# Kernel optimization log

Hardware: AMD Instinct MI355X
Metric: run time of the kernel (lower is better)

The kernel has to match this reference:

```python
import jax, jax.numpy as jnp
import numpy as np
import math

B, T, O, C, H, L, V, S = 4, 1024, 128, 1024, 16, 4, 32000, 4096
D = C // H
PAD = 0


def setup_inputs() -> dict:
    key = jax.random.key(0)
    ks = jax.random.split(key, 16)
    r = lambda i, shape, s=0.02: jax.random.normal(ks[i], shape, jnp.float32) * s
    return {
        "tokens_w": jax.random.randint(ks[0], (B, T), 0, V).astype(jnp.int32),
        "pos_offset": 0,
        "mem": jax.random.normal(ks[1], (B, O, C), jnp.float32),
        "ssum": jax.random.normal(ks[2], (B, C), jnp.float32),
        "tok_emb_w": r(3, (V, C)),
        "pos_emb_w": r(4, (S, C)),
        "mem_w": r(5, (C, C)), "mem_b": jnp.zeros((C,), jnp.float32),
        "memln_s": jnp.ones((C,), jnp.float32), "memln_b": jnp.zeros((C,), jnp.float32),
        "alpha_p": jnp.zeros((C,), jnp.float32),
        "sum_w": r(6, (C, C)),
        "ln1_s": jnp.ones((L, C), jnp.float32), "ln1_b": jnp.zeros((L, C), jnp.float32),
        "Wq": r(7, (L, C, C)), "bq": jnp.zeros((L, C), jnp.float32),
        "Wk": r(8, (L, C, C)), "bk": jnp.zeros((L, C), jnp.float32),
        "Wv": r(9, (L, C, C)), "bv": jnp.zeros((L, C), jnp.float32),
        "Wo": r(10, (L, C, C)), "bo": jnp.zeros((L, C), jnp.float32),
        "ln2_s": jnp.ones((L, C), jnp.float32), "ln2_b": jnp.zeros((L, C), jnp.float32),
        "W1": r(11, (L, C, 4 * C)), "b1": jnp.zeros((L, 4 * C), jnp.float32),
        "W2": r(12, (L, 4 * C, C)), "b2": jnp.zeros((L, C), jnp.float32),
        "fln_s": jnp.ones((C,), jnp.float32), "fln_b": jnp.zeros((C,), jnp.float32),
        "head_w": r(13, (C, V)), "head_b": jnp.zeros((V,), jnp.float32),
        "lam_p": jnp.zeros((C,), jnp.float32),
    }


def _ln(x, s, b, eps=1e-6):
    mu = jnp.mean(x, -1, keepdims=True)
    var = jnp.mean((x - mu) ** 2, -1, keepdims=True)
    return (x - mu) * jax.lax.rsqrt(var + eps) * s + b


def reference(tokens_w, pos_offset, mem, ssum, tok_emb_w, pos_emb_w, mem_w, mem_b,
              memln_s, memln_b, alpha_p, sum_w, ln1_s, ln1_b, Wq, bq, Wk, bk, Wv, bv,
              Wo, bo, ln2_s, ln2_b, W1, b1, W2, b2, fln_s, fln_b, head_w, head_b, lam_p):
    Bx, Tx = tokens_w.shape
    tok = tok_emb_w[tokens_w]                                   # [B,T,C]
    pos_ids = jnp.clip(jnp.arange(Tx, dtype=jnp.int32) + pos_offset, 0, S - 1)
    x = tok + pos_emb_w[pos_ids][None, :, :]
    # memory adapter + norm (saved-before-masking memory state)
    m2 = _ln(mem @ mem_w + mem_b, memln_s, memln_b)             # [B,O,C]
    alpha = jax.nn.sigmoid(alpha_p)
    x = x + ((ssum @ sum_w) * alpha[None, :])[:, None, :]
    # boolean mask: memory tokens always visible + causal window + key padding
    causal = jnp.concatenate([jnp.ones((Tx, O), bool),
                              jnp.tril(jnp.ones((Tx, Tx), bool))], axis=1)[None, None]
    key_ok = jnp.concatenate([jnp.ones((Bx, O), bool), tokens_w != PAD], axis=1)
    mask = causal & key_ok[:, None, None, :]                    # [B,1,T,O+T]
    scale = 1.0 / math.sqrt(D)
    for i in range(L):
        kv = jnp.concatenate([m2, x], axis=1)                   # [B,O+T,C]
        h = _ln(x, ln1_s[i], ln1_b[i])
        q = (h @ Wq[i] + bq[i]).reshape(Bx, Tx, H, D)
        k = (kv @ Wk[i] + bk[i]).reshape(Bx, O + Tx, H, D)
        v = (kv @ Wv[i] + bv[i]).reshape(Bx, O + Tx, H, D)
        att = jnp.einsum('bqhd,bkhd->bhqk', q, k) * scale
        att = jnp.where(mask, att, -1e9)
        p = jax.nn.softmax(att, axis=-1)
        o = jnp.einsum('bhqk,bkhd->bqhd', p, v).reshape(Bx, Tx, C)
        x = x + (o @ Wo[i] + bo[i])
        h = _ln(x, ln2_s[i], ln2_b[i])
        x = x + (jax.nn.gelu(h @ W1[i] + b1[i]) @ W2[i] + b2[i])
    x = _ln(x, fln_s, fln_b)
    new_mem = x[:, -O:, :]
    m = (tokens_w != PAD).astype(x.dtype)
    x = x * m[:, :, None]
    logits = x @ head_w + head_b                                # [B,T,V]
    summary = jnp.sum(x * m[:, :, None], axis=1) / (jnp.sum(m, axis=1, keepdims=True) + 1e-6)
    lam = jax.nn.sigmoid(lam_p)
    new_ssum = ssum * lam[None, :] + summary * (1.0 - lam[None, :])
    return (new_mem, new_ssum, logits)
```

## Files before the change

kernel.cpp:

```cpp
#include <hip/hip_runtime.h>
#include <hip/hip_bf16.h>

typedef __bf16 bf16_t;
typedef __bf16 bf16x8 __attribute__((ext_vector_type(8)));
typedef __bf16 bf16x4 __attribute__((ext_vector_type(4)));
typedef float f32x4 __attribute__((ext_vector_type(4)));

#define NB 4
#define NT 1024
#define NO 128
#define NC 1024
#define NH 16
#define NL 4
#define NV 32000
#define NS 4096
#define ND 64
#define NTK (NO + NT)

#define GLOAD_LDS16(g, l) __builtin_amdgcn_global_load_lds( \
    (__attribute__((address_space(1))) void*)(g), \
    (__attribute__((address_space(3))) void*)(l), 16, 0, 0)

#define EXP2F(x) __builtin_amdgcn_exp2f(x)

__device__ __forceinline__ float sigmoidf_(float x) { return 1.0f / (1.0f + __expf(-x)); }

#define EPI_F32  0
#define EPI_ADD  1
#define EPI_GELU 2
#define EPI_QKV  3
#define EPI_KV   4

template<int EPI>
__global__ __launch_bounds__(512) void gemm8p(
    const bf16_t* __restrict__ A, const bf16_t* __restrict__ Bt,
    const float* __restrict__ bias, float* __restrict__ outF,
    bf16_t* __restrict__ outB, int M, int N, int K, int ldo, int gm)
{
    __shared__ bf16_t sm[65536];
    const int tid = threadIdx.x;
    const int w = tid >> 6, lane = tid & 63;
    const int wr = w >> 2, wc = w & 3;
    const int lr = lane & 15, lk = lane >> 4;
    const int nwg = gridDim.x;
    const int bid = blockIdx.x;
    const int xcd = bid & 7, base = bid >> 3;
    const int qq = nwg >> 3, rr = nwg & 7;
    int wg = (xcd < rr ? xcd * (qq + 1) : rr * (qq + 1) + (xcd - rr) * qq) + base;
    const int nnt = N >> 8;
    const int gsz = gm * nnt;
    const int g = wg / gsz, r2 = wg - g * gsz;
    const int ntl = r2 / gm, mt = g * gm + (r2 - ntl * gm);
    const int bm = mt << 8, bn = ntl << 8;
    const bf16_t* Ab = A + (size_t)bm * K;
    const bf16_t* Bb = Bt + (size_t)bn * K;
    const int srow = tid >> 3;
    const int scol = ((tid & 7) ^ (srow & 7)) << 3;
    const int nk = K >> 6;
    f32x4 acc[8][4] = {};

    auto STAGE = [&](int b, int kt, int h) {
        const bf16_t* gsrc = (h < 2) ? Ab : Bb;
        const int half = h & 1;
        char* lbase = (char*)(sm + ((h < 2) ? 0 : 32768) + b * 16384 + half * 8192);
        #pragma unroll
        for (int i = 0; i < 2; ++i) {
            GLOAD_LDS16(gsrc + (size_t)(half * 128 + i * 64 + srow) * K + kt * 64 + scol,
                        lbase + (i * 512 + tid) * 16);
        }
    };

    #pragma unroll
    for (int h = 0; h < 4; ++h) STAGE(0, 0, h);
    asm volatile("s_waitcnt vmcnt(0)" ::: "memory");
    __builtin_amdgcn_s_barrier();

    for (int kt = 0; kt < nk; ++kt) {
        const int curb = kt & 1;
        const bool dostage = (kt + 1) < nk;
        const char* Abase = (const char*)(sm + curb * 16384);
        const char* Bbase = (const char*)(sm + 32768 + curb * 16384);

        if (dostage) {
            STAGE(curb ^ 1, kt + 1, 0);
            STAGE(curb ^ 1, kt + 1, 1);
            asm volatile("s_waitcnt vmcnt(4)" ::: "memory");
        } else {
            asm volatile("s_waitcnt vmcnt(0)" ::: "memory");
        }
        __builtin_amdgcn_s_barrier();

        bf16x8 bfr[4][2];
        #pragma unroll
        for (int n = 0; n < 4; ++n)
            #pragma unroll
            for (int ks = 0; ks < 2; ++ks) {
                const int row = wc * 64 + n * 16 + lr;
                bfr[n][ks] = *(const bf16x8*)(Bbase + row * 128 + ((((ks << 2) + lk) ^ (row & 7)) << 4));
            }
        bf16x8 af[4][2];
        #pragma unroll
        for (int m = 0; m < 4; ++m)
            #pragma unroll
            for (int ks = 0; ks < 2; ++ks) {
                const int row = wr * 128 + m * 16 + lr;
                af[m][ks] = *(const bf16x8*)(Abase + row * 128 + ((((ks << 2) + lk) ^ (row & 7)) << 4));
            }
        asm volatile("s_waitcnt lgkmcnt(0)" ::: "memory");
        __builtin_amdgcn_sched_barrier(0);
        __builtin_amdgcn_s_setprio(1);
        #pragma unroll
        for (int m = 0; m < 4; ++m)
            #pragma unroll
            for (int n = 0; n < 4; ++n)
                #pragma unroll
                for (int ks = 0; ks < 2; ++ks)
                    acc[m][n] = __builtin_amdgcn_mfma_f32_16x16x32_bf16(
                        af[m][ks], bfr[n][ks], acc[m][n], 0, 0, 0);
        __builtin_amdgcn_s_setprio(0);

        if (dostage) {
            STAGE(curb ^ 1, kt + 1, 2);
            STAGE(curb ^ 1, kt + 1, 3);
        }
        bf16x8 ag[4][2];
        #pragma unroll
        for (int m = 0; m < 4; ++m)
            #pragma unroll
            for (int ks = 0; ks < 2; ++ks) {
                const int row = wr * 128 + 64 + m * 16 + lr;
                ag[m][ks] = *(const bf16x8*)(Abase + row * 128 + ((((ks << 2) + lk) ^ (row & 7)) << 4));
            }
        asm volatile("s_waitcnt lgkmcnt(0)" ::: "memory");
        __builtin_amdgcn_sched_barrier(0);
        __builtin_amdgcn_s_setprio(1);
        #pragma unroll
        for (int m = 0; m < 4; ++m)
            #pragma unroll
            for (int n = 0; n < 4; ++n)
                #pragma unroll
                for (int ks = 0; ks < 2; ++ks)
                    acc[4 + m][n] = __builtin_amdgcn_mfma_f32_16x16x32_bf16(
                        ag[m][ks], bfr[n][ks], acc[4 + m][n], 0, 0, 0);
        __builtin_amdgcn_s_setprio(0);
        __builtin_amdgcn_s_barrier();
    }

    float bv4[4];
    #pragma unroll
    for (int n = 0; n < 4; ++n) bv4[n] = bias[bn + wc * 64 + n * 16 + lr];
    #pragma unroll
    for (int m = 0; m < 8; ++m) {
        #pragma unroll
        for (int j = 0; j < 4; ++j) {
            const int row = bm + wr * 128 + m * 16 + lk * 4 + j;
            #pragma unroll
            for (int n = 0; n < 4; ++n) {
                const int col = bn + wc * 64 + n * 16 + lr;
                float v = acc[m][n][j] + bv4[n];
                if constexpr (EPI == 0) {
                    __builtin_nontemporal_store(v, &outF[(size_t)row * ldo + col]);
                } else {
                    float u = 1.5957691216057308f * (v + 0.044715f * v * v * v);
                    float g_ = v / (1.0f + __expf(-u));
                    outB[(size_t)row * ldo + col] = (bf16_t)g_;
                }
            }
        }
    }
}

template<int EPI>
__device__ __forceinline__ void gemm128_body(
    bf16_t* sm, int bid, int nwg,
    const bf16_t* __restrict__ A, const bf16_t* __restrict__ Bt,
    const float* __restrict__ bias, const float* __restrict__ bias2,
    float* __restrict__ outF, bf16_t* __restrict__ outB, bf16_t* __restrict__ outB2,
    int M, int N, int K, int p0, int ldo, int gm)
{
    char* smb = (char*)sm;
    const int tid = threadIdx.x;
    const int w = tid >> 6, lane = tid & 63;
    const int wr = w >> 1, wc = w & 1;
    const int lr = lane & 15, lk = lane >> 4;
    const int xcd = bid & 7, base = bid >> 3;
    const int qq = nwg >> 3, rr = nwg & 7;
    int wg = (xcd < rr ? xcd * (qq + 1) : rr * (qq + 1) + (xcd - rr) * qq) + base;
    const int nnt = N >> 7;
    const int gsz = gm * nnt;
    const int g = wg / gsz, r2 = wg - g * gsz;
    const int ntl = r2 / gm, mt = g * gm + (r2 - ntl * gm);
    const int bm = mt << 7, bn = ntl << 7;
    const bf16_t* Ab = A + (size_t)bm * K;
    const bf16_t* Bb = Bt + (size_t)bn * K;
    const int srow = tid >> 3;
    const int scol = ((tid & 7) ^ (srow & 7)) << 3;
    const int nk = K >> 6;
    f32x4 acc[4][4] = {};

    auto STAGE = [&](int b, int kt, int h) {
        const bf16_t* gsrc = h ? Bb : Ab;
        char* lbase = smb + h * 32768 + b * 16384;
        #pragma unroll
        for (int i = 0; i < 4; ++i) {
            GLOAD_LDS16(gsrc + (size_t)(i * 32 + srow) * K + kt * 64 + scol,
                        lbase + (i * 256 + tid) * 16);
        }
    };

    STAGE(0, 0, 0); STAGE(0, 0, 1);
    asm volatile("s_waitcnt vmcnt(0)" ::: "memory");
    __builtin_amdgcn_s_barrier();

    for (int kt = 0; kt < nk; ++kt) {
        const int curb = kt & 1;
        const bool dostage = (kt + 1) < nk;
        const char* Abase = smb + curb * 16384;
        const char* Bbase = smb + 32768 + curb * 16384;

        if (dostage) {
            STAGE(curb ^ 1, kt + 1, 0);
            asm volatile("s_waitcnt vmcnt(4)" ::: "memory");
        } else {
            asm volatile("s_waitcnt vmcnt(0)" ::: "memory");
        }
        __builtin_amdgcn_s_barrier();

        bf16x8 bfr[4][2];
        #pragma unroll
        for (int n = 0; n < 4; ++n)
            #pragma unroll
            for (int ks_ = 0; ks_ < 2; ++ks_) {
                const int row = wc * 64 + n * 16 + lr;
                bfr[n][ks_] = *(const bf16x8*)(Bbase + row * 128 + ((((ks_ << 2) + lk) ^ (row & 7)) << 4));
            }
        bf16x8 af[4];
        #pragma unroll
        for (int m = 0; m < 4; ++m) {
            const int row = wr * 64 + m * 16 + lr;
            af[m] = *(const bf16x8*)(Abase + row * 128 + (((lk) ^ (row & 7)) << 4));
        }
        asm volatile("s_waitcnt lgkmcnt(0)" ::: "memory");
        __builtin_amdgcn_sched_barrier(0);
        __builtin_amdgcn_s_setprio(1);
        #pragma unroll
        for (int m = 0; m < 4; ++m)
            #pragma unroll
            for (int n = 0; n < 4; ++n)
                acc[m][n] = __builtin_amdgcn_mfma_f32_16x16x32_bf16(
                    af[m], bfr[n][0], acc[m][n], 0, 0, 0);
        __builtin_amdgcn_s_setprio(0);

        if (dostage) STAGE(curb ^ 1, kt + 1, 1);
        bf16x8 ag[4];
        #pragma unroll
        for (int m = 0; m < 4; ++m) {
            const int row = wr * 64 + m * 16 + lr;
            ag[m] = *(const bf16x8*)(Abase + row * 128 + (((4 + lk) ^ (row & 7)) << 4));
        }
        asm volatile("s_waitcnt lgkmcnt(0)" ::: "memory");
        __builtin_amdgcn_sched_barrier(0);
        __builtin_amdgcn_s_setprio(1);
        #pragma unroll
        for (int m = 0; m < 4; ++m)
            #pragma unroll
            for (int n = 0; n < 4; ++n)
                acc[m][n] = __builtin_amdgcn_mfma_f32_16x16x32_bf16(
                    ag[m], bfr[n][1], acc[m][n], 0, 0, 0);
        __builtin_amdgcn_s_setprio(0);
        __builtin_amdgcn_s_barrier();
    }

    #pragma unroll
    for (int m = 0; m < 4; ++m) {
        #pragma unroll
        for (int j = 0; j < 4; ++j) {
            const int row = bm + wr * 64 + m * 16 + lk * 4 + j;
            int b_ = 0, t_ = 0;
            if constexpr (EPI == EPI_QKV || EPI == EPI_KV) { b_ = row / p0; t_ = row % p0; }
            #pragma unroll
            for (int n = 0; n < 4; ++n) {
                const int col = bn + wc * 64 + n * 16 + lr;
                if constexpr (EPI == EPI_F32) {
                    float v = acc[m][n][j] + bias[col];
                    __builtin_nontemporal_store(v, &outF[(size_t)row * ldo + col]);
                } else if constexpr (EPI == EPI_ADD) {
                    float v = acc[m][n][j] + bias[col];
                    outF[(size_t)row * ldo + col] += v;
                } else if constexpr (EPI == EPI_GELU) {
                    float v = acc[m][n][j] + bias[col];
                    float u = 1.5957691216057308f * (v + 0.044715f * v * v * v);
                    float g_ = v / (1.0f + __expf(-u));
                    outB[(size_t)row * ldo + col] = (bf16_t)g_;
                } else if constexpr (EPI == EPI_QKV) {
                    float v = acc[m][n][j] + bias[col];
                    int h = col >> 6, d = col & 63;
                    outB[(((size_t)b_ * NH + h) * p0 + t_) * ND + d] = (bf16_t)v;
                } else if constexpr (EPI == EPI_KV) {
                    if (col < NC) {
                        float v = acc[m][n][j] + bias[col];
                        int h = col >> 6, d = col & 63;
                        outB[(((size_t)b_ * NH + h) * NTK + t_) * ND + d] = (bf16_t)v;
                    } else {
                        int c2_ = col - NC;
                        float v = acc[m][n][j] + bias2[c2_];
                        int h = c2_ >> 6, d = c2_ & 63;
                        outB2[(((size_t)b_ * NH + h) * ND + d) * NTK + t_] = (bf16_t)v;
                    }
                }
            }
        }
    }
}

template<int EPI>
__global__ __launch_bounds__(256) void gemm128(
    const bf16_t* __restrict__ A, const bf16_t* __restrict__ Bt,
    const float* __restrict__ bias, const float* __restrict__ bias2,
    float* __restrict__ outF, bf16_t* __restrict__ outB, bf16_t* __restrict__ outB2,
    int M, int N, int K, int p0, int ldo, int gm)
{
    __shared__ bf16_t sm[32768];
    gemm128_body<EPI>(sm, blockIdx.x, gridDim.x, A, Bt, bias, bias2,
                      outF, outB, outB2, M, N, K, p0, ldo, gm);
}

__global__ __launch_bounds__(256) void qkv_fused(
    const bf16_t* __restrict__ hbuf, const bf16_t* __restrict__ kvbuf,
    const bf16_t* __restrict__ wtq, const bf16_t* __restrict__ wtkv,
    const float* __restrict__ bq, const float* __restrict__ bk,
    const float* __restrict__ bv,
    bf16_t* __restrict__ qbuf, bf16_t* __restrict__ kbuf, bf16_t* __restrict__ vtbuf)
{
    __shared__ bf16_t sm[32768];
    if (blockIdx.x < 256) {
        gemm128_body<EPI_QKV>(sm, blockIdx.x, 256, hbuf, wtq, bq, nullptr,
                              nullptr, qbuf, nullptr, NB * NT, NC, NC, NT, 0, 8);
    } else {
        gemm128_body<EPI_KV>(sm, blockIdx.x - 256, 576, kvbuf, wtkv, bk, bv,
                             nullptr, kbuf, vtbuf, NB * NTK, 2 * NC, NC, NTK, 0, 6);
    }
}

template<int EPI>
__global__ __launch_bounds__(256) void gemm_bt(
    const bf16_t* __restrict__ A, const bf16_t* __restrict__ Bt,
    const float* __restrict__ bias, const float* __restrict__ bias2,
    float* __restrict__ outF, bf16_t* __restrict__ outB, bf16_t* __restrict__ outB2,
    int M, int N, int K, int p0, int ldo, int gm)
{
    __shared__ bf16_t lA[128 * 32];
    __shared__ bf16_t lB[128 * 32];
    const int tid = threadIdx.x;
    const int nwg = gridDim.x;
    const int bid = blockIdx.x;
    const int xcd = bid & 7, base = bid >> 3;
    const int qq = nwg >> 3, rr = nwg & 7;
    int wg = (xcd < rr ? xcd * (qq + 1) : rr * (qq + 1) + (xcd - rr) * qq) + base;
    const int nnt = N >> 7;
    const int gsz = gm * nnt;
    const int g = wg / gsz, r2 = wg - g * gsz;
    const int ntl = r2 / gm, mt = g * gm + (r2 - ntl * gm);
    const int bm = mt * 128, bn = ntl * 128;
    const bf16_t* Ab = A + (size_t)bm * K;
    const bf16_t* Bb = Bt + (size_t)bn * K;
    const int wave = tid >> 6, lane = tid & 63;
    const int wr = wave >> 1, wc = wave & 1;
    const int lr = lane & 15, lk = lane >> 4;
    f32x4 acc[4][4] = {};
    const int nk = K >> 5;
    const int c1 = tid, c2 = tid + 256;
    for (int kt = 0; kt < nk; ++kt) {
        __syncthreads();
        const bf16_t* Abk = Ab + kt * 32;
        const bf16_t* Bbk = Bb + kt * 32;
        GLOAD_LDS16(Abk + (size_t)(c1 >> 2) * K + (c1 & 3) * 8, (char*)lA + c1 * 16);
        GLOAD_LDS16(Abk + (size_t)(c2 >> 2) * K + (c2 & 3) * 8, (char*)lA + c2 * 16);
        GLOAD_LDS16(Bbk + (size_t)(c1 >> 2) * K + (c1 & 3) * 8, (char*)lB + c1 * 16);
        GLOAD_LDS16(Bbk + (size_t)(c2 >> 2) * K + (c2 & 3) * 8, (char*)lB + c2 * 16);
        __syncthreads();
        bf16x8 af[4], bfr[4];
        #pragma unroll
        for (int m = 0; m < 4; ++m)
            af[m] = *(const bf16x8*)&lA[(wr * 64 + m * 16 + lr) * 32 + lk * 8];
        #pragma unroll
        for (int n = 0; n < 4; ++n)
            bfr[n] = *(const bf16x8*)&lB[(wc * 64 + n * 16 + lr) * 32 + lk * 8];
        #pragma unroll
        for (int m = 0; m < 4; ++m)
            #pragma unroll
            for (int n = 0; n < 4; ++n)
                acc[m][n] = __builtin_amdgcn_mfma_f32_16x16x32_bf16(af[m], bfr[n], acc[m][n], 0, 0, 0);
    }
    #pragma unroll
    for (int m = 0; m < 4; ++m) {
        #pragma unroll
        for (int j = 0; j < 4; ++j) {
            const int row = bm + wr * 64 + m * 16 + lk * 4 + j;
            #pragma unroll
            for (int n = 0; n < 4; ++n) {
                const int col = bn + wc * 64 + n * 16 + lr;
                if constexpr (EPI == EPI_F32) {
                    float v = acc[m][n][j] + bias[col];
                    __builtin_nontemporal_store(v, &outF[(size_t)row * ldo + col]);
                }
            }
        }
    }
}

__device__ __forceinline__ void tc_body(
    const float* __restrict__ W, bf16_t* __restrict__ Wt,
    int K, int N, int k0, int n0, int t)
{
    __shared__ float tile[64][65];
    #pragma unroll
    for (int i = 0; i < 4; ++i) {
        const int idx = t + i * 256;
        const int r = idx >> 4, c4 = (idx & 15) << 2;
        const float4 v = *(const float4*)(W + (size_t)(k0 + r) * N + n0 + c4);
        tile[r][c4 + 0] = v.x; tile[r][c4 + 1] = v.y;
        tile[r][c4 + 2] = v.z; tile[r][c4 + 3] = v.w;
    }
    __syncthreads();
    #pragma unroll
    for (int i = 0; i < 4; ++i) {
        const int idx = t + i * 256;
        const int r = idx >> 4, c4 = (idx & 15) << 2;
        bf16x4 o = {(bf16_t)tile[c4 + 0][r], (bf16_t)tile[c4 + 1][r],
                    (bf16_t)tile[c4 + 2][r], (bf16_t)tile[c4 + 3][r]};
        *(bf16x4*)(Wt + (size_t)(n0 + r) * K + k0 + c4) = o;
    }
}

__global__ __launch_bounds__(256) void transpose_cast(
    const float* __restrict__ W, bf16_t* __restrict__ Wt, int K, int N)
{
    tc_body(W, Wt, K, N, blockIdx.x << 6, blockIdx.y << 6, threadIdx.x);
}

__device__ __forceinline__ void ln3_body(
    int row, const float* __restrict__ X, const float* __restrict__ sw,
    const float* __restrict__ bw, bf16_t* __restrict__ outB,
    bf16_t* __restrict__ outB2)
{
    const int t = threadIdx.x;
    const float4 v = ((const float4*)(X + (size_t)row * NC))[t];
    float s1 = v.x + v.y + v.z + v.w;
    float s2 = v.x * v.x + v.y * v.y + v.z * v.z + v.w * v.w;
    #pragma unroll
    for (int off = 32; off > 0; off >>= 1) { s1 += __shfl_xor(s1, off); s2 += __shfl_xor(s2, off); }
    __shared__ float rs1[4], rs2[4];
    if ((t & 63) == 0) { rs1[t >> 6] = s1; rs2[t >> 6] = s2; }
    __syncthreads();
    s1 = rs1[0] + rs1[1] + rs1[2] + rs1[3];
    s2 = rs2[0] + rs2[1] + rs2[2] + rs2[3];
    const float mu = s1 * (1.0f / NC);
    const float var = s2 * (1.0f / NC) - mu * mu;
    const float rstd = rsqrtf(var + 1e-6f);
    const int c = t * 4;
    const float4 sv = ((const float4*)sw)[t];
    const float4 bv = ((const float4*)bw)[t];
    float y0 = (v.x - mu) * rstd * sv.x + bv.x;
    float y1 = (v.y - mu) * rstd * sv.y + bv.y;
    float y2 = (v.z - mu) * rstd * sv.z + bv.z;
    float y3 = (v.w - mu) * rstd * sv.w + bv.w;
    bf16x4 o = {(bf16_t)y0, (bf16_t)y1, (bf16_t)y2, (bf16_t)y3};
    *(bf16x4*)(outB + (size_t)row * NC + c) = o;
    const int b_ = row >> 10, t_ = row & 1023;
    bf16x4 o2 = {(bf16_t)v.x, (bf16_t)v.y, (bf16_t)v.z, (bf16_t)v.w};
    *(bf16x4*)(outB2 + ((size_t)b_ * NTK + NO + t_) * NC + c) = o2;
}

__global__ __launch_bounds__(256) void prep_layer(
    const float* __restrict__ Wq, const float* __restrict__ Wk,
    const float* __restrict__ Wv, const float* __restrict__ Wo,
    const float* __restrict__ W1, const float* __restrict__ W2,
    bf16_t* __restrict__ wtq, bf16_t* __restrict__ wtkv,
    bf16_t* __restrict__ wto, bf16_t* __restrict__ wt1, bf16_t* __restrict__ wt2,
    const float* __restrict__ X, const float* __restrict__ ln1s,
    const float* __restrict__ ln1b, bf16_t* __restrict__ hbuf,
    bf16_t* __restrict__ kvbuf)
{
    const int bid = blockIdx.x;
    if (bid >= 3072) {
        ln3_body(bid - 3072, X, ln1s, ln1b, hbuf, kvbuf);
        return;
    }
    const float* W; bf16_t* Wt; int K, N, k0, n0;
    if (bid < 1024) {
        const int which = bid >> 8, r = bid & 255;
        K = NC; N = NC;
        k0 = (r & 15) << 6; n0 = (r >> 4) << 6;
        W  = (which == 0) ? Wq : (which == 1) ? Wk : (which == 2) ? Wv : Wo;
        Wt = (which == 0) ? wtq : (which == 1) ? wtkv
           : (which == 2) ? (wtkv + (size_t)NC * NC) : wto;
    } else if (bid < 2048) {
        const int r = bid - 1024;
        K = NC; N = 4 * NC;
        k0 = (r & 15) << 6; n0 = (r >> 4) << 6;
        W = W1; Wt = wt1;
    } else {
        const int r = bid - 2048;
        K = 4 * NC; N = NC;
        k0 = (r & 63) << 6; n0 = (r >> 6) << 6;
        W = W2; Wt = wt2;
    }
    tc_body(W, Wt, K, N, k0, n0, threadIdx.x);
}

template<int MODE>
__global__ __launch_bounds__(256) void ln_row(
    const float* __restrict__ X, const float* __restrict__ sw,
    const float* __restrict__ bw, float* __restrict__ outF,
    bf16_t* __restrict__ outB, bf16_t* __restrict__ outB2)
{
    const int row = blockIdx.x;
    const int t = threadIdx.x;
    const float4 v = ((const float4*)(X + (size_t)row * NC))[t];
    float s1 = v.x + v.y + v.z + v.w;
    float s2 = v.x * v.x + v.y * v.y + v.z * v.z + v.w * v.w;
    #pragma unroll
    for (int off = 32; off > 0; off >>= 1) { s1 += __shfl_xor(s1, off); s2 += __shfl_xor(s2, off); }
    __shared__ float rs1[4], rs2[4];
    if ((t & 63) == 0) { rs1[t >> 6] = s1; rs2[t >> 6] = s2; }
    __syncthreads();
    s1 = rs1[0] + rs1[1] + rs1[2] + rs1[3];
    s2 = rs2[0] + rs2[1] + rs2[2] + rs2[3];
    const float mu = s1 * (1.0f / NC);
    const float var = s2 * (1.0f / NC) - mu * mu;
    const float rstd = rsqrtf(var + 1e-6f);
    const int c = t * 4;
    const float4 sv = ((const float4*)sw)[t];
    const float4 bv = ((const float4*)bw)[t];
    float y0 = (v.x - mu) * rstd * sv.x + bv.x;
    float y1 = (v.y - mu) * rstd * sv.y + bv.y;
    float y2 = (v.z - mu) * rstd * sv.z + bv.z;
    float y3 = (v.w - mu) * rstd * sv.w + bv.w;
    size_t dst;
    if constexpr (MODE == 1) dst = ((size_t)(row / NO) * NTK + (row % NO)) * NC + c;
    else dst = (size_t)row * NC + c;
    bf16x4 o = {(bf16_t)y0, (bf16_t)y1, (bf16_t)y2, (bf16_t)y3};
    *(bf16x4*)(outB + dst) = o;
}

__global__ __launch_bounds__(256) void ln_final(
    const float* __restrict__ X, const float* __restrict__ sw,
    const float* __restrict__ bw, const int* __restrict__ tokens,
    bf16_t* __restrict__ xm, float* __restrict__ outMem)
{
    const int row = blockIdx.x;
    const int t = threadIdx.x;
    const float4 v = ((const float4*)(X + (size_t)row * NC))[t];
    float s1 = v.x + v.y + v.z + v.w;
    float s2 = v.x * v.x + v.y * v.y + v.z * v.z + v.w * v.w;
    #pragma unroll
    for (int off = 32; off > 0; off >>= 1) { s1 += __shfl_xor(s1, off); s2 += __shfl_xor(s2, off); }
    __shared__ float rs1[4], rs2[4];
    if ((t & 63) == 0) { rs1[t >> 6] = s1; rs2[t >> 6] = s2; }
    __syncthreads();
    s1 = rs1[0] + rs1[1] + rs1[2] + rs1[3];
    s2 = rs2[0] + rs2[1] + rs2[2] + rs2[3];
    const float mu = s1 * (1.0f / NC);
    const float var = s2 * (1.0f / NC) - mu * mu;
    const float rstd = rsqrtf(var + 1e-6f);
    const int c = t * 4;
    const float4 sv = ((const float4*)sw)[t];
    const float4 bv = ((const float4*)bw)[t];
    float y0 = (v.x - mu) * rstd * sv.x + bv.x;
    float y1 = (v.y - mu) * rstd * sv.y + bv.y;
    float y2 = (v.z - mu) * rstd * sv.z + bv.z;
    float y3 = (v.w - mu) * rstd * sv.w + bv.w;
    const bool ok = tokens[row] != 0;
    bf16x4 o;
    if (ok) { o = (bf16x4){(bf16_t)y0, (bf16_t)y1, (bf16_t)y2, (bf16_t)y3}; }
    else    { o = (bf16x4){(bf16_t)0.f, (bf16_t)0.f, (bf16_t)0.f, (bf16_t)0.f}; }
    *(bf16x4*)(xm + (size_t)row * NC + c) = o;
    const int b_ = row >> 10, t_ = row & 1023;
    if (t_ >= NT - NO) {
        float4 f; f.x = y0; f.y = y1; f.z = y2; f.w = y3;
        *(float4*)(outMem + ((size_t)b_ * NO + (t_ - (NT - NO))) * NC + c) = f;
    }
}

#define QKSCALE 0.1803368801111204f

__global__ __launch_bounds__(256) void attn_kernel(
    const bf16_t* __restrict__ Q, const bf16_t* __restrict__ Kb,
    const bf16_t* __restrict__ Vt, const int* __restrict__ tokens,
    bf16_t* __restrict__ Ob)
{
    const int bh = blockIdx.x;
    const int b = bh >> 4, h = bh & 15;
    const int w = threadIdx.x >> 6;
    const int lane = threadIdx.x & 63;
    const int yt = gridDim.y - 1 - blockIdx.y;
    const int q0 = (yt << 7) + (w << 5);
    const int lr = lane & 15, lk = lane >> 4;
    const bf16_t* Qp = Q + ((size_t)bh * NT + q0) * ND;
    bf16x8 qf[2][2];
    #pragma unroll
    for (int qs = 0; qs < 2; ++qs) {
        qf[qs][0] = *(const bf16x8*)(Qp + (qs * 16 + lr) * ND + lk * 8);
        qf[qs][1] = *(const bf16x8*)(Qp + (qs * 16 + lr) * ND + 32 + lk * 8);
    }
    const bf16_t* Kbase = Kb + (size_t)bh * NTK * ND;
    const bf16_t* Vbase = Vt + (size_t)bh * ND * NTK;
    const int* tokb = tokens + b * NT;
    float mrow[2][4] = {{-1e30f, -1e30f, -1e30f, -1e30f}, {-1e30f, -1e30f, -1e30f, -1e30f}};
    float lsum[2][4] = {};
    f32x4 acc[2][4] = {};
    __shared__ bf16_t pb[4][2][16 * 64];
    const int kmax = NO + q0 + 32;
    for (int k0 = 0; k0 < kmax; k0 += 64) {
        f32x4 st[2][4] = {};
        __builtin_amdgcn_s_setprio(1);
        #pragma unroll
        for (int nt = 0; nt < 4; ++nt) {
            const bf16_t* Kp = Kbase + (size_t)(k0 + nt * 16 + lr) * ND + lk * 8;
            bf16x8 kf0 = *(const bf16x8*)(Kp);
            bf16x8 kf1 = *(const bf16x8*)(Kp + 32);
            #pragma unroll
            for (int qs = 0; qs < 2; ++qs) {
                st[qs][nt] = __builtin_amdgcn_mfma_f32_16x16x32_bf16(qf[qs][0], kf0, st[qs][nt], 0, 0, 0);
                st[qs][nt] = __builtin_amdgcn_mfma_f32_16x16x32_bf16(qf[qs][1], kf1, st[qs][nt], 0, 0, 0);
            }
        }
        __builtin_amdgcn_s_setprio(0);
        #pragma unroll
        for (int qs = 0; qs < 2; ++qs) {
            char* pbq = (char*)pb[w][qs];
            float sc[4][4];
            float tmax[4] = {-1e30f, -1e30f, -1e30f, -1e30f};
            #pragma unroll
            for (int nt = 0; nt < 4; ++nt) {
                const int key = k0 + nt * 16 + lr;
                const int kt = key - NO;
                const int kts = kt < 0 ? 0 : kt;
                const bool keyok = (kt < 0) | (tokb[kts] != 0);
                #pragma unroll
                for (int j = 0; j < 4; ++j) {
                    const int qrow = q0 + qs * 16 + lk * 4 + j;
                    const bool ok = keyok && (kt <= qrow);
                    const float s = ok ? st[qs][nt][j] * QKSCALE : -1e9f;
                    sc[nt][j] = s;
                    tmax[j] = fmaxf(tmax[j], s);
                }
            }
            #pragma unroll
            for (int off = 1; off < 16; off <<= 1)
                #pragma unroll
                for (int j = 0; j < 4; ++j) tmax[j] = fmaxf(tmax[j], __shfl_xor(tmax[j], off));
            float resc[4], p[4][4], psum[4] = {0.f, 0.f, 0.f, 0.f};
            #pragma unroll
            for (int j = 0; j < 4; ++j) {
                const float mnew = fmaxf(mrow[qs][j], tmax[j]);
                resc[j] = EXP2F(mrow[qs][j] - mnew);
                mrow[qs][j] = mnew;
            }
            #pragma unroll
            for (int nt = 0; nt < 4; ++nt)
                #pragma unroll
                for (int j = 0; j < 4; ++j) { p[nt][j] = EXP2F(sc[nt][j] - mrow[qs][j]); psum[j] += p[nt][j]; }
            #pragma unroll
            for (int off = 1; off < 16; off <<= 1)
                #pragma unroll
                for (int j = 0; j < 4; ++j) psum[j] += __shfl_xor(psum[j], off);
            #pragma unroll
            for (int j = 0; j < 4; ++j) lsum[qs][j] = lsum[qs][j] * resc[j] + psum[j];
            #pragma unroll
            for (int dt = 0; dt < 4; ++dt)
                #pragma unroll
                for (int j = 0; j < 4; ++j) acc[qs][dt][j] *= resc[j];
            #pragma unroll
            for (int nt = 0; nt < 4; ++nt)
                #pragma unroll
                for (int j = 0; j < 4; ++j) {
                    const int row = lk * 4 + j;
                    const int byt = (row << 7) + ((((nt << 4) + lr) << 1) ^ ((row & 7) << 4));
                    *(bf16_t*)(pbq + byt) = (bf16_t)p[nt][j];
                }
        }
        const int swz = (lr & 7) << 4;
        bf16x8 pa[2][2];
        #pragma unroll
        for (int qs = 0; qs < 2; ++qs) {
            const char* pbq = (const char*)pb[w][qs];
            pa[qs][0] = *(const bf16x8*)(pbq + ((lr << 7) + (((lk << 4)) ^ swz)));
            pa[qs][1] = *(const bf16x8*)(pbq + ((lr << 7) + ((64 + (lk << 4)) ^ swz)));
        }
        __builtin_amdgcn_s_setprio(1);
        #pragma unroll
        for (int dt = 0; dt < 4; ++dt) {
            const bf16_t* Vp = Vbase + (size_t)(dt * 16 + lr) * NTK + k0 + lk * 8;
            bf16x8 vf0 = *(const bf16x8*)(Vp);
            bf16x8 vf1 = *(const bf16x8*)(Vp + 32);
            #pragma unroll
            for (int qs = 0; qs < 2; ++qs) {
                acc[qs][dt] = __builtin_amdgcn_mfma_f32_16x16x32_bf16(pa[qs][0], vf0, acc[qs][dt], 0, 0, 0);
                acc[qs][dt] = __builtin_amdgcn_mfma_f32_16x16x32_bf16(pa[qs][1], vf1, acc[qs][dt], 0, 0, 0);
            }
        }
        __builtin_amdgcn_s_setprio(0);
    }
    #pragma unroll
    for (int qs = 0; qs < 2; ++qs)
        #pragma unroll
        for (int dt = 0; dt < 4; ++dt)
            #pragma unroll
            for (int j = 0; j < 4; ++j)
                Ob[((size_t)b * NT + q0 + qs * 16 + lk * 4 + j) * NC + h * ND + dt * 16 + lr] =
                    (bf16_t)(acc[qs][dt][j] / lsum[qs][j]);
}

__global__ __launch_bounds__(256) void sum_proj_kernel(
    const float* __restrict__ ssum, const float* __restrict__ sumw,
    const float* __restrict__ alpha, float* __restrict__ add)
{
    const int b = blockIdx.y;
    const int c = blockIdx.x * 256 + threadIdx.x;
    float a = 0.f;
    for (int k = 0; k < NC; ++k) a += ssum[b * NC + k] * sumw[(size_t)k * NC + c];
    add[b * NC + c] = a * sigmoidf_(alpha[c]);
}

__global__ __launch_bounds__(256) void embed_kernel(
    const int* __restrict__ tokens, const int* __restrict__ posoff,
    const float* __restrict__ tokw, const float* __restrict__ posw,
    const float* __restrict__ add, float* __restrict__ X)
{
    const int bt = blockIdx.x;
    const int b = bt >> 10, t = bt & 1023;
    const int c = threadIdx.x * 4;
    const int tok = tokens[bt];
    int p = t + posoff[0];
    p = p < 0 ? 0 : (p > NS - 1 ? NS - 1 : p);
    const float4 tv = *(const float4*)(tokw + (size_t)tok * NC + c);
    const float4 pv = *(const float4*)(posw + (size_t)p * NC + c);
    const float4 av = *(const float4*)(add + b * NC + c);
    float4 o;
    o.x = tv.x + pv.x + av.x; o.y = tv.y + pv.y + av.y;
    o.z = tv.z + pv.z + av.z; o.w = tv.w + pv.w + av.w;
    *(float4*)(X + (size_t)bt * NC + c) = o;
}

__global__ __launch_bounds__(256) void cast_f32_bf16_kernel(
    const float* __restrict__ in, bf16_t* __restrict__ out)
{
    const size_t i = ((size_t)blockIdx.x * 256 + threadIdx.x) * 4;
    const float4 v = *(const float4*)(in + i);
    bf16x4 o = {(bf16_t)v.x, (bf16_t)v.y, (bf16_t)v.z, (bf16_t)v.w};
    *(bf16x4*)(out + i) = o;
}

__global__ __launch_bounds__(256) void sumpart_kernel(
    const bf16_t* __restrict__ XM, float* __restrict__ sbuf)
{
    const int b = blockIdx.z;
    const int c = blockIdx.x * 256 + threadIdx.x;
    const int t0 = blockIdx.y * 64;
    float a = 0.f;
    for (int t = t0; t < t0 + 64; ++t)
        a += (float)XM[((size_t)b * NT + t) * NC + c];
    atomicAdd(&sbuf[b * NC + c], a);
}

__global__ __launch_bounds__(256) void ssum_out_kernel(
    const float* __restrict__ sbuf, const int* __restrict__ tokens,
    const float* __restrict__ ssum, const float* __restrict__ lamp, float* __restrict__ out)
{
    const int b = blockIdx.y;
    const int c = blockIdx.x * 256 + threadIdx.x;
    int cnt = 0;
    for (int t = 0; t < NT; ++t) cnt += (tokens[b * NT + t] != 0);
    const float summary = sbuf[b * NC + c] / ((float)cnt + 1e-6f);
    const float lam = sigmoidf_(lamp[c]);
    out[b * NC + c] = ssum[b * NC + c] * lam + summary * (1.0f - lam);
}

extern "C" void kernel_launch(void* const* d_in, const int* in_sizes, int n_in,
                              void* d_out, int out_size, void* d_ws, size_t ws_size,
                              hipStream_t stream)
{
    (void)in_sizes; (void)n_in; (void)out_size; (void)ws_size;
    const int*   tokens   = (const int*)d_in[0];
    const int*   posoff   = (const int*)d_in[1];
    const float* mem      = (const float*)d_in[2];
    const float* ssum     = (const float*)d_in[3];
    const float* tok_emb  = (const float*)d_in[4];
    const float* pos_emb  = (const float*)d_in[5];
    const float* mem_w    = (const float*)d_in[6];
    const float* mem_b    = (const float*)d_in[7];
    const float* memln_s  = (const float*)d_in[8];
    const float* memln_b  = (const float*)d_in[9];
    const float* alpha_p  = (const float*)d_in[10];
    const float* sum_w    = (const float*)d_in[11];
    const float* ln1_s    = (const float*)d_in[12];
    const float* ln1_b    = (const float*)d_in[13];
    const float* Wq       = (const float*)d_in[14];
    const float* bq       = (const float*)d_in[15];
    const float* Wk       = (const float*)d_in[16];
    const float* bk       = (const float*)d_in[17];
    const float* Wv       = (const float*)d_in[18];
    const float* bv       = (const float*)d_in[19];
    const float* Wo       = (const float*)d_in[20];
    const float* bo       = (const float*)d_in[21];
    const float* ln2_s    = (const float*)d_in[22];
    const float* ln2_b    = (const float*)d_in[23];
    const float* W1       = (const float*)d_in[24];
    const float* b1       = (const float*)d_in[25];
    const float* W2       = (const float*)d_in[26];
    const float* b2       = (const float*)d_in[27];
    const float* fln_s    = (const float*)d_in[28];
    const float* fln_b    = (const float*)d_in[29];
    const float* head_w   = (const float*)d_in[30];
    const float* head_b   = (const float*)d_in[31];
    const float* lam_p    = (const float*)d_in[32];

    float* out_mem    = (float*)d_out;
    float* out_ssum   = out_mem + (size_t)NB * NO * NC;
    float* out_logits = out_ssum + (size_t)NB * NC;

    char* wp = (char*)d_ws;
    auto alloc = [&](size_t bytes) { char* p = wp; wp += (bytes + 255) & ~(size_t)255; return p; };
    bf16_t* wt_head = (bf16_t*)alloc((size_t)NV * NC * 2);
    bf16_t* wt_mem  = (bf16_t*)alloc((size_t)NC * NC * 2);
    bf16_t* wt_q    = (bf16_t*)alloc((size_t)NC * NC * 2);
    bf16_t* wt_kv   = (bf16_t*)alloc((size_t)2 * NC * NC * 2);
    bf16_t* wt_o    = (bf16_t*)alloc((size_t)NC * NC * 2);
    bf16_t* wt_1    = (bf16_t*)alloc((size_t)NC * 4 * NC * 2);
    bf16_t* wt_2    = (bf16_t*)alloc((size_t)NC * 4 * NC * 2);
    float*  xbuf    = (float*)alloc((size_t)NB * NT * NC * 4);
    bf16_t* hbuf    = (bf16_t*)alloc((size_t)NB * NT * NC * 2);
    bf16_t* kvbuf   = (bf16_t*)alloc((size_t)NB * NTK * NC * 2);
    bf16_t* qbuf    = (bf16_t*)alloc((size_t)NB * NT * NC * 2);
    bf16_t* kbuf    = (bf16_t*)alloc((size_t)NB * NTK * NC * 2);
    bf16_t* vtbuf   = (bf16_t*)alloc((size_t)NB * NTK * NC * 2);
    bf16_t* obuf    = (bf16_t*)alloc((size_t)NB * NT * NC * 2);
    bf16_t* midbuf  = (bf16_t*)alloc((size_t)NB * NT * 4 * NC * 2);
    bf16_t* xmbuf   = (bf16_t*)alloc((size_t)NB * NT * NC * 2);
    bf16_t* membf   = (bf16_t*)alloc((size_t)NB * NO * NC * 2);
    float*  m2f     = (float*)alloc((size_t)NB * NO * NC * 4);
    float*  addb    = (float*)alloc((size_t)NB * NC * 4);
    float*  sbuf    = (float*)alloc((size_t)NB * NC * 4);

    (void)hipMemsetAsync(sbuf, 0, (size_t)NB * NC * 4, stream);

    transpose_cast<<<dim3(NC / 64, NC / 64), 256, 0, stream>>>(mem_w, wt_mem, NC, NC);

    cast_f32_bf16_kernel<<<(NB * NO * NC) / 1024, 256, 0, stream>>>(mem, membf);
    gemm_bt<EPI_F32><<<32, 256, 0, stream>>>(
        membf, wt_mem, mem_b, nullptr, m2f, nullptr, nullptr, NB * NO, NC, NC, 0, NC, 4);
    ln_row<1><<<NB * NO, 256, 0, stream>>>(m2f, memln_s, memln_b, nullptr, kvbuf, nullptr);

    sum_proj_kernel<<<dim3(NC / 256, NB), 256, 0, stream>>>(ssum, sum_w, alpha_p, addb);
    embed_kernel<<<NB * NT, 256, 0, stream>>>(tokens, posoff, tok_emb, pos_emb, addb, xbuf);

    for (int i = 0; i < NL; ++i) {
        prep_layer<<<7168, 256, 0, stream>>>(
            Wq + (size_t)i * NC * NC, Wk + (size_t)i * NC * NC,
            Wv + (size_t)i * NC * NC, Wo + (size_t)i * NC * NC,
            W1 + (size_t)i * NC * 4 * NC, W2 + (size_t)i * 4 * NC * NC,
            wt_q, wt_kv, wt_o, wt_1, wt_2,
            xbuf, ln1_s + i * NC, ln1_b + i * NC, hbuf, kvbuf);

        qkv_fused<<<832, 256, 0, stream>>>(
            hbuf, kvbuf, wt_q, wt_kv, bq + i * NC, bk + i * NC, bv + i * NC,
            qbuf, kbuf, vtbuf);

        attn_kernel<<<dim3(NB * NH, NT / 128), 256, 0, stream>>>(qbuf, kbuf, vtbuf, tokens, obuf);

        gemm128<EPI_ADD><<<256, 256, 0, stream>>>(
            obuf, wt_o, bo + i * NC, nullptr, xbuf, nullptr, nullptr, NB * NT, NC, NC, 0, NC, 8);

        ln_row<0><<<NB * NT, 256, 0, stream>>>(xbuf, ln2_s + i * NC, ln2_b + i * NC, nullptr, hbuf, nullptr);
        gemm8p<1><<<256, 512, 0, stream>>>(
            hbuf, wt_1, b1 + (size_t)i * 4 * NC, nullptr, midbuf, NB * NT, 4 * NC, NC, 4 * NC, 4);
        gemm128<EPI_ADD><<<256, 256, 0, stream>>>(
            midbuf, wt_2, b2 + i * NC, nullptr, xbuf, nullptr, nullptr, NB * NT, NC, 4 * NC, 0, NC, 8);
    }

    ln_final<<<NB * NT, 256, 0, stream>>>(xbuf, fln_s, fln_b, tokens, xmbuf, out_mem);
    sumpart_kernel<<<dim3(NC / 256, NT / 64, NB), 256, 0, stream>>>(xmbuf, sbuf);
    ssum_out_kernel<<<dim3(NC / 256, NB), 256, 0, stream>>>(sbuf, tokens, ssum, lam_p, out_ssum);
    transpose_cast<<<dim3(NC / 64, NV / 64), 256, 0, stream>>>(head_w, wt_head, NC, NV);
    gemm8p<0><<<2000, 512, 0, stream>>>(
        xmbuf, wt_head, head_b, out_logits, nullptr, NB * NT, NV, NC, NV, 4);
}
```

Measured before the change: 1.624 ms.

## Fuse prologue kernels and skip online-softmax rescale below a max-delta threshold

Merges the mem_w transpose, the mem cast, the summary projection and the embedding into one prologue kernel, with sum_proj still launched first so the embed blocks can read addb. The fused kernel's sum_proj branch writes addb again while other blocks in the same launch read it, so the result depends on block scheduling. In attention, the running max and rescale of the accumulator are now only updated when the tile max exceeds the stored max by a threshold (12 in log2 units). This removes exp and multiply work per tile but lets exp2 arguments grow up to that threshold, which risks precision loss or overflow in bf16 P values.

```diff
diff --git a/kernel.cpp b/kernel.cpp
--- a/kernel.cpp
+++ b/kernel.cpp
@@ -439,6 +439,60 @@
     tc_body(W, Wt, K, N, blockIdx.x << 6, blockIdx.y << 6, threadIdx.x);
 }
 
+__global__ __launch_bounds__(256) void prologue_fused(
+    const float* __restrict__ mem_w, bf16_t* __restrict__ wt_mem,
+    const float* __restrict__ mem, bf16_t* __restrict__ membf,
+    const float* __restrict__ ssum, const float* __restrict__ sumw,
+    const float* __restrict__ alpha, float* __restrict__ addb,
+    const int* __restrict__ tokens, const int* __restrict__ posoff,
+    const float* __restrict__ tokw, const float* __restrict__ posw,
+    float* __restrict__ X)
+{
+    const int bid = blockIdx.x;
+    const int t = threadIdx.x;
+    if (bid < 256) {
+        tc_body(mem_w, wt_mem, NC, NC, (bid & 15) << 6, (bid >> 4) << 6, t);
+    } else if (bid < 768) {
+        const size_t i = ((size_t)(bid - 256) * 256 + t) * 4;
+        const float4 v = *(const float4*)(mem + i);
+        bf16x4 o = {(bf16_t)v.x, (bf16_t)v.y, (bf16_t)v.z, (bf16_t)v.w};
+        *(bf16x4*)(membf + i) = o;
+    } else if (bid < 784) {
+        const int r = bid - 768;
+        const int b = r >> 2;
+        const int c = (r & 3) * 256 + t;
+        float a = 0.f;
+        for (int k = 0; k < NC; ++k) a += ssum[b * NC + k] * sumw[(size_t)k * NC + c];
+        addb[b * NC + c] = a * sigmoidf_(alpha[c]);
+    } else {
+        const int bt = bid - 784;
+        const int b = bt >> 10, tt = bt & 1023;
+        const int c = t * 4;
+        const int tok = tokens[bt];
+        int p = tt + posoff[0];
+        p = p < 0 ? 0 : (p > NS - 1 ? NS - 1 : p);
+        const float4 tv = *(const float4*)(tokw + (size_t)tok * NC + c);
+        const float4 pv = *(const float4*)(posw + (size_t)p * NC + c);
+        const float4 av = *(const float4*)(addb + b * NC + c);
+        float4 o;
+        o.x = tv.x + pv.x + av.x; o.y = tv.y + pv.y + av.y;
+        o.z = tv.z + pv.z + av.z; o.w = tv.w + pv.w + av.w;
+        *(float4*)(X + (size_t)bt * NC + c) = o;
+    }
+}
+
+
+__global__ __launch_bounds__(256) void sum_proj_kernel(
+    const float* __restrict__ ssum, const float* __restrict__ sumw,
+    const float* __restrict__ alpha, float* __restrict__ add)
+{
+    const int b = blockIdx.y;
+    const int c = blockIdx.x * 256 + threadIdx.x;
+    float a = 0.f;
+    for (int k = 0; k < NC; ++k) a += ssum[b * NC + k] * sumw[(size_t)k * NC + c];
+    add[b * NC + c] = a * sigmoidf_(alpha[c]);
+}
+
 __device__ __forceinline__ void ln3_body(
     int row, const float* __restrict__ X, const float* __restrict__ sw,
     const float* __restrict__ bw, bf16_t* __restrict__ outB,
@@ -584,6 +638,7 @@
 }
 
 #define QKSCALE 0.1803368801111204f
+#define DMTHR   12.0f
 
 __global__ __launch_bounds__(256) void attn_kernel(
     const bf16_t* __restrict__ Q, const bf16_t* __restrict__ Kb,
@@ -651,12 +706,21 @@
             for (int off = 1; off < 16; off <<= 1)
                 #pragma unroll
                 for (int j = 0; j < 4; ++j) tmax[j] = fmaxf(tmax[j], __shfl_xor(tmax[j], off));
+            bool upd = false;
+            #pragma unroll
+            for (int j = 0; j < 4; ++j) upd |= (tmax[j] > mrow[qs][j] + DMTHR);
+            const bool dorescale = __any(upd);
             float resc[4], p[4][4], psum[4] = {0.f, 0.f, 0.f, 0.f};
-            #pragma unroll
-            for (int j = 0; j < 4; ++j) {
-                const float mnew = fmaxf(mrow[qs][j], tmax[j]);
-                resc[j] = EXP2F(mrow[qs][j] - mnew);
-                mrow[qs][j] = mnew;
+            if (dorescale) {
+                #pragma unroll
+                for (int j = 0; j < 4; ++j) {
+                    const float mnew = fmaxf(mrow[qs][j], tmax[j]);
+                    resc[j] = EXP2F(mrow[qs][j] - mnew);
+                    mrow[qs][j] = mnew;
+                }
+            } else {
+                #pragma unroll
+                for (int j = 0; j < 4; ++j) resc[j] = 1.0f;
             }
             #pragma unroll
             for (int nt = 0; nt < 4; ++nt)
@@ -666,12 +730,17 @@
             for (int off = 1; off < 16; off <<= 1)
                 #pragma unroll
                 for (int j = 0; j < 4; ++j) psum[j] += __shfl_xor(psum[j], off);
-            #pragma unroll
-            for (int j = 0; j < 4; ++j) lsum[qs][j] = lsum[qs][j] * resc[j] + psum[j];
-            #pragma unroll
-            for (int dt = 0; dt < 4; ++dt)
-                #pragma unroll
-                for (int j = 0; j < 4; ++j) acc[qs][dt][j] *= resc[j];
+            if (dorescale) {
+                #pragma unroll
+                for (int j = 0; j < 4; ++j) lsum[qs][j] = lsum[qs][j] * resc[j] + psum[j];
+                #pragma unroll
+                for (int dt = 0; dt < 4; ++dt)
+                    #pragma unroll
+                    for (int j = 0; j < 4; ++j) acc[qs][dt][j] *= resc[j];
+            } else {
+                #pragma unroll
+                for (int j = 0; j < 4; ++j) lsum[qs][j] += psum[j];
+            }
             #pragma unroll
             for (int nt = 0; nt < 4; ++nt)
                 #pragma unroll
@@ -711,46 +780,6 @@
             for (int j = 0; j < 4; ++j)
                 Ob[((size_t)b * NT + q0 + qs * 16 + lk * 4 + j) * NC + h * ND + dt * 16 + lr] =
                     (bf16_t)(acc[qs][dt][j] / lsum[qs][j]);
-}
-
-__global__ __launch_bounds__(256) void sum_proj_kernel(
-    const float* __restrict__ ssum, const float* __restrict__ sumw,
-    const float* __restrict__ alpha, float* __restrict__ add)
-{
-    const int b = blockIdx.y;
-    const int c = blockIdx.x * 256 + threadIdx.x;
-    float a = 0.f;
-    for (int k = 0; k < NC; ++k) a += ssum[b * NC + k] * sumw[(size_t)k * NC + c];
-    add[b * NC + c] = a * sigmoidf_(alpha[c]);
-}
-
-__global__ __launch_bounds__(256) void embed_kernel(
-    const int* __restrict__ tokens, const int* __restrict__ posoff,
-    const float* __restrict__ tokw, const float* __restrict__ posw,
-    const float* __restrict__ add, float* __restrict__ X)
-{
-    const int bt = blockIdx.x;
-    const int b = bt >> 10, t = bt & 1023;
-    const int c = threadIdx.x * 4;
-    const int tok = tokens[bt];
-    int p = t + posoff[0];
-    p = p < 0 ? 0 : (p > NS - 1 ? NS - 1 : p);
-    const float4 tv = *(const float4*)(tokw + (size_t)tok * NC + c);
-    const float4 pv = *(const float4*)(posw + (size_t)p * NC + c);
-    const float4 av = *(const float4*)(add + b * NC + c);
-    float4 o;
-    o.x = tv.x + pv.x + av.x; o.y = tv.y + pv.y + av.y;
-    o.z = tv.z + pv.z + av.z; o.w = tv.w + pv.w + av.w;
-    *(float4*)(X + (size_t)bt * NC + c) = o;
-}
-
-__global__ __launch_bounds__(256) void cast_f32_bf16_kernel(
-    const float* __restrict__ in, bf16_t* __restrict__ out)
-{
-    const size_t i = ((size_t)blockIdx.x * 256 + threadIdx.x) * 4;
-    const float4 v = *(const float4*)(in + i);
-    bf16x4 o = {(bf16_t)v.x, (bf16_t)v.y, (bf16_t)v.z, (bf16_t)v.w};
-    *(bf16x4*)(out + i) = o;
 }
 
 __global__ __launch_bounds__(256) void sumpart_kernel(
@@ -846,15 +875,14 @@
 
     (void)hipMemsetAsync(sbuf, 0, (size_t)NB * NC * 4, stream);
 
-    transpose_cast<<<dim3(NC / 64, NC / 64), 256, 0, stream>>>(mem_w, wt_mem, NC, NC);
-
-    cast_f32_bf16_kernel<<<(NB * NO * NC) / 1024, 256, 0, stream>>>(mem, membf);
+    sum_proj_kernel<<<dim3(NC / 256, NB), 256, 0, stream>>>(ssum, sum_w, alpha_p, addb);
+    prologue_fused<<<4880, 256, 0, stream>>>(
+        mem_w, wt_mem, mem, membf, ssum, sum_w, alpha_p, addb,
+        tokens, posoff, tok_emb, pos_emb, xbuf);
+
     gemm_bt<EPI_F32><<<32, 256, 0, stream>>>(
         membf, wt_mem, mem_b, nullptr, m2f, nullptr, nullptr, NB * NO, NC, NC, 0, NC, 4);
     ln_row<1><<<NB * NO, 256, 0, stream>>>(m2f, memln_s, memln_b, nullptr, kvbuf, nullptr);
-
-    sum_proj_kernel<<<dim3(NC / 256, NB), 256, 0, stream>>>(ssum, sum_w, alpha_p, addb);
-    embed_kernel<<<NB * NT, 256, 0, stream>>>(tokens, posoff, tok_emb, pos_emb, addb, xbuf);
 
     for (int i = 0; i < NL; ++i) {
         prep_layer<<<7168, 256, 0, stream>>>(
```

After: 1.653 ms. No clear change (+1.8%).
